# Performance work log

Measured on AMD Instinct MI355X. Metric: run time of the kernel, lower is better.

## Reference

```python
import jax, jax.numpy as jnp
import numpy as np
from jax import lax

# dims from the TED skeleton used by speech2affective_gestures
N, T, J, C = 256, 1024, 9, 3      # batch, frames, directed edges (graph1 nodes), coords
K1, K2 = 5, 3                     # spatial partitions of A1, A2
F1, F2 = 16, 16                   # st_gcn output channels
NUM_PARTS, MAX_EDGES = 3, 3       # body parts, edges per part
BODY_PARTS = np.array([[0, 1, 2], [3, 4, 5], [6, 7, 8]])  # body_parts_edge_idx
EPS = 1e-5
LEAK = 0.01


def conv2d_nchw(x, w):
    kh = w.shape[2]
    return lax.conv_general_dilated(x, w, (1, 1), ((kh // 2, kh // 2), (0, 0)),
                                    dimension_numbers=("NCHW", "OIHW", "NCHW"))


def conv1d_nch(x, w):
    k = w.shape[2]
    return lax.conv_general_dilated(x, w, (1,), ((k // 2, k // 2),),
                                    dimension_numbers=("NCH", "OIH", "NCH"))


def bn1d(x, w, b, m, v):
    # inference-mode BatchNorm1d over channel axis 1 of (N, C, T)
    scale = w / jnp.sqrt(v + EPS)
    return x * scale[None, :, None] + (b - m * scale)[None, :, None]


def leaky(x):
    return jnp.where(x > 0, x, LEAK * x)


def setup_inputs() -> dict:
    key = jax.random.key(0)
    ks = jax.random.split(key, 12)
    s = 0.05
    return {
        "poses": jax.random.normal(ks[0], (N, T, J * C), jnp.float32),
        "A1": jax.random.uniform(ks[1], (K1, J, J), jnp.float32) / J,
        "A2": jax.random.uniform(ks[2], (K2, NUM_PARTS, NUM_PARTS), jnp.float32) / NUM_PARTS,
        "W1": jax.random.normal(ks[3], (F1 * K1, C, 9, 1), jnp.float32) * s,
        "b1": jnp.zeros((F1 * K1,), jnp.float32),
        "W2": jax.random.normal(ks[4], (F2 * K2, MAX_EDGES * F1, 9, 1), jnp.float32) * s,
        "b2": jnp.zeros((F2 * K2,), jnp.float32),
        "Wc1": jax.random.normal(ks[5], (16, F2 * NUM_PARTS, 5), jnp.float32) * s,
        "bc1": jnp.zeros((16,), jnp.float32),
        "bn1_w": jnp.ones((16,), jnp.float32), "bn1_b": jnp.zeros((16,), jnp.float32),
        "bn1_m": jnp.zeros((16,), jnp.float32), "bn1_v": jnp.ones((16,), jnp.float32),
        "Wc2": jax.random.normal(ks[6], (8, 16, 3), jnp.float32) * s,
        "bc2": jnp.zeros((8,), jnp.float32),
        "bn2_w": jnp.ones((8,), jnp.float32), "bn2_b": jnp.zeros((8,), jnp.float32),
        "bn2_m": jnp.zeros((8,), jnp.float32), "bn2_v": jnp.ones((8,), jnp.float32),
    }


def reference(poses, A1, A2, W1, b1, W2, b2, Wc1, bc1, bn1_w, bn1_b, bn1_m, bn1_v,
              Wc2, bc2, bn2_w, bn2_b, bn2_m, bn2_v):
    n, t, jc = poses.shape
    x = jnp.transpose(poses.reshape(n, t, J, C), (0, 3, 1, 2))  # (n, 3, t, 9)

    # st_gcn1: temporal conv -> split K partitions -> graph contraction with A1
    y = conv2d_nchw(x, W1) + b1[None, :, None, None]            # (n, K1*F1, t, 9)
    y = y.reshape(n, K1, F1, t, J)
    feat1 = jnp.einsum("nkctv,kvw->nctw", y, A1)                # (n, 16, t, 9)

    # body-part gather/pack: feat2_in channel layout is (c slow, edge fast)
    g = feat1[:, :, :, BODY_PARTS]                              # (n, 16, t, parts, edges)
    feat2_in = jnp.transpose(g, (0, 1, 4, 2, 3)).reshape(n, F1 * MAX_EDGES, t, NUM_PARTS)

    # st_gcn2
    y2 = conv2d_nchw(feat2_in, W2) + b2[None, :, None, None]    # (n, K2*F2, t, 3)
    y2 = y2.reshape(n, K2, F2, t, NUM_PARTS)
    feat2 = jnp.einsum("nkctv,kvw->nctw", y2, A2)               # (n, 16, t, 3)

    # flatten (c, v) with c slow -> (n, 48, t)
    feat3_in = jnp.transpose(feat2, (0, 1, 3, 2)).reshape(n, F2 * NUM_PARTS, t)

    h = leaky(bn1d(conv1d_nch(feat3_in, Wc1) + bc1[None, :, None], bn1_w, bn1_b, bn1_m, bn1_v))
    h = leaky(bn1d(conv1d_nch(h, Wc2) + bc2[None, :, None], bn2_w, bn2_b, bn2_m, bn2_v))
    return jnp.transpose(h, (0, 2, 1))                          # (n, t, 8)
```

## Files before the change

### kernel.cpp

```cpp
#include <hip/hip_runtime.h>

namespace {
constexpr int T_ = 1024;
constexpr int NBATCH = 256;

constexpr int WFB_OFF    = 0;
constexpr int WFC_OFF    = 82944;
constexpr int WFD_OFF    = 221184;
constexpr int WBIG_OFF   = 231424;
constexpr int WFE_OFF    = 252928;
constexpr int BIASB_OFF  = 254976;
constexpr int BIASC_OFF  = 255552;
constexpr int BIASD_OFF  = 255744;
constexpr int BIASBIG_OFF= 255808;
constexpr int BIASE_OFF  = 255872;
constexpr int WCOMP_OFF  = 262144;

constexpr int R0 = 41472;
constexpr int R1 = R0 + 69120;
constexpr int R2 = R1 + 5120;
constexpr int R3 = R2 + 1024;
constexpr int R4 = R3 + 29952;
constexpr int R5 = R4 + 144;
constexpr int R6 = R5 + 48;
constexpr int R7 = R6 + 16;
constexpr int R8 = R7 + 8;

constexpr int SLAB_OFF  = 0;
constexpr int H1_OFF    = 18688;
constexpr int TT_FX     = 50;
constexpr int FXF2IN    = 0;
constexpr int FXF3      = FXF2IN + 72 * 320;
constexpr int FXSLAB    = FXF3 + 68 * 144;
constexpr int FXH1      = FXSLAB;
constexpr int SMEM_FUSE = FXSLAB + 72 * 80;
static_assert(SMEM_FUSE <= 65536, "fused LDS");

typedef __attribute__((ext_vector_type(8))) short short8v;
typedef __attribute__((ext_vector_type(4))) float f32x4;

__device__ inline unsigned short f2b(float f) {
  union { float f; unsigned u; } v; v.f = f;
  unsigned r = (v.u + 0x7FFFu + ((v.u >> 16) & 1u)) >> 16;
  return (unsigned short)r;
}
__device__ inline float b2f(unsigned short u) {
  union { unsigned u; float f; } v; v.u = ((unsigned)u) << 16;
  return v.f;
}
__device__ inline int fx_f2in_byte(int row, int slot, int within) {
  return FXF2IN + row * 320 + ((slot ^ ((row >> 2) & 3)) << 4) + within;
}
}

__global__ __launch_bounds__(256) void prep1_kernel(
    const float* __restrict__ A1, const float* __restrict__ A2,
    const float* __restrict__ W1, const float* __restrict__ b1,
    const float* __restrict__ W2, const float* __restrict__ b2,
    const float* __restrict__ Wc1, const float* __restrict__ bc1,
    const float* __restrict__ bn1w, const float* __restrict__ bn1b,
    const float* __restrict__ bn1m, const float* __restrict__ bn1v,
    const float* __restrict__ Wc2, const float* __restrict__ bc2,
    const float* __restrict__ bn2w, const float* __restrict__ bn2b,
    const float* __restrict__ bn2m, const float* __restrict__ bn2v,
    unsigned char* __restrict__ ws) {
  unsigned short* wfB = (unsigned short*)(ws + WFB_OFF);
  unsigned short* wfC = (unsigned short*)(ws + WFC_OFF);
  unsigned short* wfD = (unsigned short*)(ws + WFD_OFF);
  unsigned short* wfE = (unsigned short*)(ws + WFE_OFF);
  float* biasB = (float*)(ws + BIASB_OFF);
  float* biasC = (float*)(ws + BIASC_OFF);
  float* biasD = (float*)(ws + BIASD_OFF);
  float* biasE = (float*)(ws + BIASE_OFF);
  float* wcomp = (float*)(ws + WCOMP_OFF);
  for (int idx = blockIdx.x * 256 + threadIdx.x; idx < R8; idx += gridDim.x * 256) {
    if (idx < R0) {
      int ncol = idx / 288, k = idx - ncol * 288;
      int dh = k >> 5, mm = k & 31;
      float val = 0.f;
      if (mm < 27) {
        int v = mm / 3, ci = mm - v * 3;
        int p = ncol / 48, rr = ncol - p * 48, c = rr / 3, e = rr - c * 3;
        int w = p * 3 + e;
        for (int k5 = 0; k5 < 5; ++k5)
          val += W1[(k5 * 16 + c) * 27 + ci * 9 + dh] * A1[k5 * 81 + v * 9 + w];
      }
      wfB[idx] = f2b(val);
    } else if (idx < R1) {
      int i2 = idx - R0;
      int nc = i2 / 1440, k = i2 - nc * 1440;
      int dh = k / 160, off = k - dh * 160;
      float val = 0.f;
      if (off < 144) {
        int p = off / 48, ci2 = off - p * 48;
        int c2 = nc / 3, w2 = nc - c2 * 3;
        for (int k2 = 0; k2 < 3; ++k2)
          val += W2[(k2 * 16 + c2) * 432 + ci2 * 9 + dh] * A2[k2 * 9 + p * 3 + w2];
      }
      wfC[i2] = f2b(val);
    } else if (idx < R2) {
      int i3 = idx - R1;
      int o3 = i3 / 320, k = i3 - o3 * 320;
      int d = k >> 6, nc = k & 63;
      float val = 0.f;
      if (nc < 48) {
        float s1 = bn1w[o3] * rsqrtf(bn1v[o3] + 1e-5f);
        val = Wc1[o3 * 240 + nc * 5 + d] * s1;
      }
      wfD[i3] = f2b(val);
    } else if (idx < R3) {
      int i4 = idx - R2;
      int o4 = i4 >> 6, k = i4 & 63;
      float val = 0.f;
      if (o4 < 8 && k < 48) {
        int d = k >> 4, ci = k & 15;
        float s2 = bn2w[o4] * rsqrtf(bn2v[o4] + 1e-5f);
        val = Wc2[(o4 * 16 + ci) * 3 + d] * s2;
      }
      wfE[i4] = f2b(val);
    } else if (idx < R4) {
      int i5 = idx - R3;
      int o3 = i5 / 1872, rem = i5 - o3 * 1872;
      int dh2 = rem / 144, ncol = rem - dh2 * 144;
      int p = ncol / 48, ci2 = ncol - p * 48;
      float s1 = bn1w[o3] * rsqrtf(bn1v[o3] + 1e-5f);
      float acc = 0.f;
      for (int d = 0; d < 5; ++d) {
        int dh = dh2 - d;
        if (dh < 0 || dh > 8) continue;
        float wd = 0.f;
        for (int nc = 0; nc < 48; ++nc) {
          int c2 = nc / 3, w2 = nc - c2 * 3;
          float wc = 0.f;
          for (int k2 = 0; k2 < 3; ++k2)
            wc += W2[(k2 * 16 + c2) * 432 + ci2 * 9 + dh] * A2[k2 * 9 + p * 3 + w2];
          wd += Wc1[o3 * 240 + nc * 5 + d] * wc;
        }
        acc += wd * s1;
      }
      wcomp[i5] = acc;
    } else if (idx < R5) {
      int ib = idx - R4;
      int p = ib / 48, rr = ib - p * 48, c = rr / 3, e = rr - c * 3;
      int w = p * 3 + e;
      float val = 0.f;
      for (int k5 = 0; k5 < 5; ++k5)
        for (int v = 0; v < 9; ++v)
          val += b1[k5 * 16 + c] * A1[k5 * 81 + v * 9 + w];
      biasB[ib] = val;
    } else if (idx < R6) {
      int nc = idx - R5, c2 = nc / 3, w2 = nc - c2 * 3;
      float val = 0.f;
      for (int k2 = 0; k2 < 3; ++k2)
        for (int p = 0; p < 3; ++p)
          val += b2[k2 * 16 + c2] * A2[k2 * 9 + p * 3 + w2];
      biasC[nc] = val;
    } else if (idx < R7) {
      int o3 = idx - R6;
      float s1 = bn1w[o3] * rsqrtf(bn1v[o3] + 1e-5f);
      biasD[o3] = bc1[o3] * s1 + bn1b[o3] - bn1m[o3] * s1;
    } else {
      int o4 = idx - R7;
      float s2 = bn2w[o4] * rsqrtf(bn2v[o4] + 1e-5f);
      biasE[o4] = bc2[o4] * s2 + bn2b[o4] - bn2m[o4] * s2;
    }
  }
}

__global__ __launch_bounds__(256) void prep2_kernel(
    const float* __restrict__ Wc1, const float* __restrict__ bn1w,
    const float* __restrict__ bn1v, unsigned char* __restrict__ ws) {
  __shared__ float stgf[48 * 288];
  __shared__ float wl[1872];
  __shared__ float pr[256];
  __shared__ float pbias[192];
  const int dt = blockIdx.x, o3 = blockIdx.y;
  const int tid = threadIdx.x;
  const int m1 = tid & 31, p = tid >> 5;
  const unsigned short* wfB = (const unsigned short*)(ws + WFB_OFF);
  const float* wcomp = (const float*)(ws + WCOMP_OFF);
  unsigned short* wBIG = (unsigned short*)(ws + WBIG_OFF);

  for (int i = tid; i < 1872; i += 256) wl[i] = wcomp[o3 * 1872 + i];

  const int lo = (dt - 8) > 0 ? (dt - 8) : 0;
  const int hi = (dt < 12) ? dt : 12;
  float acc = 0.f;
  for (int c = 0; c < 3; ++c) {
    __syncthreads();
    for (int i = tid; i < 48 * 288; i += 256)
      stgf[i] = b2f(wfB[c * 13824 + i]);
    __syncthreads();
    for (int dh2 = lo; dh2 <= hi; ++dh2) {
      const int dh1 = dt - dh2;
      const float* wr = wl + dh2 * 144 + c * 48 + p * 6;
      const float* br = stgf + (p * 6) * 288 + dh1 * 32 + m1;
#pragma unroll
      for (int j = 0; j < 6; ++j)
        acc += wr[j] * br[j * 288];
    }
  }
  pr[tid] = acc;
  __syncthreads();
  if (tid < 32) {
    float s = pr[tid];
#pragma unroll
    for (int pp = 1; pp < 8; ++pp) s += pr[pp * 32 + tid];
    wBIG[o3 * 672 + dt * 32 + tid] = f2b(s);
  }
  if (dt == 0) {
    if (tid < 144) {
      float s = 0.f;
      for (int dh2 = 0; dh2 < 13; ++dh2) s += wl[dh2 * 144 + tid];
      pbias[tid] = s * ((const float*)(ws + BIASB_OFF))[tid];
    } else if (tid < 192) {
      int nc = tid - 144;
      float s1 = bn1w[o3] * rsqrtf(bn1v[o3] + 1e-5f);
      float s = 0.f;
#pragma unroll
      for (int d = 0; d < 5; ++d) s += Wc1[o3 * 240 + nc * 5 + d];
      pbias[tid] = s * s1 * ((const float*)(ws + BIASC_OFF))[nc];
    }
    __syncthreads();
    if (tid == 0) {
      float accb = ((const float*)(ws + BIASD_OFF))[o3];
      for (int i = 0; i < 192; ++i) accb += pbias[i];
      ((float*)(ws + BIASBIG_OFF))[o3] = accb;
    }
  }
}

__global__ __launch_bounds__(256, 3) void fused_kernel(
    const float* __restrict__ poses,
    const float* __restrict__ Wc2, const float* __restrict__ bc2,
    const float* __restrict__ bn2w, const float* __restrict__ bn2b,
    const float* __restrict__ bn2m, const float* __restrict__ bn2v,
    const unsigned char* __restrict__ ws, float* __restrict__ out) {
  __shared__ __attribute__((aligned(16))) unsigned char smem[SMEM_FUSE];
  const int tid = threadIdx.x;
  const int n = blockIdx.y;
  const int w = tid >> 6, l = tid & 63, lrow = l & 15, q = l >> 4, q8 = q * 8;

  if (blockIdx.x < 4) {
    const int t0 = blockIdx.x * 256;
    {
      unsigned* s32 = (unsigned*)(smem + SLAB_OFF);
      for (int idx = tid; idx < 292 * 16; idx += 256) {
        int r = idx >> 4, mi = idx & 15, m0 = mi * 2;
        int t = t0 - 18 + r;
        float v0 = 0.f, v1 = 0.f;
        if (t >= 0 && t < T_) {
          const float* src = poses + ((long)n * T_ + t) * 27;
          if (m0 < 27) v0 = src[m0];
          if (m0 + 1 < 27) v1 = src[m0 + 1];
        }
        s32[idx] = (unsigned)f2b(v0) | ((unsigned)f2b(v1) << 16);
      }
    }

    const float bb = ((const float*)(ws + BIASBIG_OFF))[lrow];
    const float be = ((const float*)(ws + BIASE_OFF))[lrow & 7];
    const unsigned short* wbg = (const unsigned short*)(ws + WBIG_OFF);
    short8v B[21];
#pragma unroll
    for (int dt = 0; dt < 21; ++dt)
      B[dt] = *(const short8v*)(wbg + lrow * 672 + dt * 32 + q8);
    const unsigned short* wfe = (const unsigned short*)(ws + WFE_OFF);
    const short8v E0 = *(const short8v*)(wfe + lrow * 64 + q8);
    const short8v E1 = *(const short8v*)(wfe + lrow * 64 + 32 + q8);
    __syncthreads();

#pragma unroll
    for (int i = 0; i < 5; ++i) {
      if (i == 4 && w != 0) continue;
      const int mt = (i < 4) ? (w + i * 4) : 16;
      const int sbase = SLAB_OFF + (mt * 16 + lrow) * 64 + q8 * 2;
      f32x4 c0 = {0.f, 0.f, 0.f, 0.f}, c1 = {0.f, 0.f, 0.f, 0.f};
      short8v a[7];
#pragma unroll
      for (int dt = 0; dt < 7; ++dt) a[dt] = *(const short8v*)(smem + sbase + dt * 64);
#pragma unroll
      for (int dt = 0; dt < 7; ++dt) {
        if (dt & 1) c1 = __builtin_amdgcn_mfma_f32_16x16x32_bf16(a[dt], B[dt], c1, 0, 0, 0);
        else        c0 = __builtin_amdgcn_mfma_f32_16x16x32_bf16(a[dt], B[dt], c0, 0, 0, 0);
      }
#pragma unroll
      for (int dt = 0; dt < 7; ++dt) a[dt] = *(const short8v*)(smem + sbase + (7 + dt) * 64);
#pragma unroll
      for (int dt = 0; dt < 7; ++dt) {
        if (dt & 1) c1 = __builtin_amdgcn_mfma_f32_16x16x32_bf16(a[dt], B[7 + dt], c1, 0, 0, 0);
        else        c0 = __builtin_amdgcn_mfma_f32_16x16x32_bf16(a[dt], B[7 + dt], c0, 0, 0, 0);
      }
#pragma unroll
      for (int dt = 0; dt < 7; ++dt) a[dt] = *(const short8v*)(smem + sbase + (14 + dt) * 64);
#pragma unroll
      for (int dt = 0; dt < 7; ++dt) {
        if (dt & 1) c1 = __builtin_amdgcn_mfma_f32_16x16x32_bf16(a[dt], B[14 + dt], c1, 0, 0, 0);
        else        c0 = __builtin_amdgcn_mfma_f32_16x16x32_bf16(a[dt], B[14 + dt], c0, 0, 0, 0);
      }
      const int hbase = H1_OFF + (mt * 16 + q * 4) * 32 + lrow * 2;
#pragma unroll
      for (int jj = 0; jj < 4; ++jj) {
        float x = c0[jj] + c1[jj] + bb;
        float h = x > 0.f ? x : 0.01f * x;
        *(unsigned short*)(smem + hbase + jj * 32) = f2b(h);
      }
    }
    __syncthreads();

#pragma unroll
    for (int i = 0; i < 4; ++i) {
      const int mte = w + i * 4;
      const int abase = H1_OFF + (7 + mte * 16 + lrow) * 32 + q8 * 2;
      short8v A0v = *(const short8v*)(smem + abase);
      short8v A1v = *(const short8v*)(smem + abase + 64);
      f32x4 acc = {0.f, 0.f, 0.f, 0.f};
      acc = __builtin_amdgcn_mfma_f32_16x16x32_bf16(A0v, E0, acc, 0, 0, 0);
      acc = __builtin_amdgcn_mfma_f32_16x16x32_bf16(A1v, E1, acc, 0, 0, 0);
      if (lrow < 8) {
        const int tb = t0 + mte * 16 + q * 4;
#pragma unroll
        for (int jj = 0; jj < 4; ++jj) {
          const int t = tb + jj;
          if (t >= 7 && t < 1017) {
            float x = acc[jj] + be;
            out[((long)n * T_ + t) * 8 + lrow] = x > 0.f ? x : 0.01f * x;
          }
        }
      }
    }
    return;
  }

  const unsigned short* wfB = (const unsigned short*)(ws + WFB_OFF);
  const unsigned short* wfC = (const unsigned short*)(ws + WFC_OFF);
  const unsigned short* wfD = (const unsigned short*)(ws + WFD_OFF);
  const float* biasB = (const float*)(ws + BIASB_OFF);
  const float* biasC = (const float*)(ws + BIASC_OFF);
  const float* biasD = (const float*)(ws + BIASD_OFF);
  const int e = blockIdx.x - 4;
  const int t0 = e ? (T_ - TT_FX) : 0;

  {
    unsigned* slab32 = (unsigned*)(smem + FXSLAB);
    for (int it = tid; it < 72 * 20; it += 256) {
      int r = it / 20, mi = it - r * 20;
      int t = t0 - 11 + r;
      int m0 = mi * 2;
      float v0 = 0.f, v1 = 0.f;
      if (t >= 0 && t < T_) {
        const float* src = poses + ((long)n * T_ + t) * 27;
        if (m0 < 27) v0 = src[m0];
        if (m0 + 1 < 27) v1 = src[m0 + 1];
      }
      slab32[it] = (unsigned)f2b(v0) | ((unsigned)f2b(v1) << 16);
    }
    for (int it = tid; it < 64 * 8; it += 256) {
      int r = it >> 3, u = it & 7;
      int s = 18 + (u >> 2);
      *(unsigned*)(smem + fx_f2in_byte(r, s, (u & 3) * 4)) = 0;
    }
    for (int it = tid; it < 8 * 80; it += 256) {
      int r = 64 + it / 80, u = it - (it / 80) * 80;
      *(unsigned*)(smem + FXF2IN + r * 320 + u * 4) = 0;
    }
    for (int it = tid; it < 68 * 8 + 12 * 24; it += 256) {
      if (it < 68 * 8) {
        int r = it >> 3, u = it & 7;
        *(unsigned*)(smem + FXF3 + r * 144 + 96 + u * 4) = 0;
      } else {
        int k2 = it - 68 * 8;
        int r = 56 + k2 / 24, u = k2 - (k2 / 24) * 24;
        *(unsigned*)(smem + FXF3 + r * 144 + u * 4) = 0;
      }
    }
  }
  __syncthreads();

  {
    const int ntS = (w == 0) ? 0 : (2 * w + 1);
    const int ntN = (w == 0) ? 3 : 2;
#pragma unroll
    for (int ni = 0; ni < 3; ++ni) {
      if (ni < ntN) {
        const int nt = ntS + ni;
        short8v b[9];
#pragma unroll
        for (int dh = 0; dh < 9; ++dh)
          b[dh] = *(const short8v*)(wfB + (nt * 16 + lrow) * 288 + dh * 32 + q8);
        const int ncol = nt * 16 + lrow;
        const float bias = biasB[ncol];
#pragma unroll
        for (int mt = 0; mt < 4; ++mt) {
          short8v a[9];
#pragma unroll
          for (int dh = 0; dh < 9; ++dh)
            a[dh] = *(const short8v*)(smem + FXSLAB + ((mt * 16 + lrow + dh) * 40 + q8) * 2);
          f32x4 c0 = {0.f, 0.f, 0.f, 0.f}, c1 = {0.f, 0.f, 0.f, 0.f};
#pragma unroll
          for (int dh = 0; dh < 9; ++dh) {
            if (dh & 1) c1 = __builtin_amdgcn_mfma_f32_16x16x32_bf16(a[dh], b[dh], c1, 0, 0, 0);
            else        c0 = __builtin_amdgcn_mfma_f32_16x16x32_bf16(a[dh], b[dh], c0, 0, 0, 0);
          }
#pragma unroll
          for (int jj = 0; jj < 4; ++jj) {
            const int r = mt * 16 + q * 4 + jj;
            const int t = t0 - 7 + r;
            float v = (t >= 0 && t < T_) ? c0[jj] + c1[jj] + bias : 0.f;
            *(unsigned short*)(smem + fx_f2in_byte(r, ncol >> 3, (ncol & 7) * 2)) = f2b(v);
          }
        }
      }
    }
  }
  __syncthreads();

  if (w < 3) {
    const int ncol2 = w * 16 + lrow;
    const float bias = biasC[ncol2];
    f32x4 acc[4];
#pragma unroll
    for (int mt = 0; mt < 4; ++mt) acc[mt] = {0.f, 0.f, 0.f, 0.f};
#pragma unroll
    for (int g = 0; g < 5; ++g) {
      short8v b[9];
#pragma unroll
      for (int i = 0; i < 9; ++i) {
        const int kf = g * 9 + i, dh = kf / 5, kkl = kf % 5;
        b[i] = *(const short8v*)(wfC + ncol2 * 1440 + dh * 160 + kkl * 32 + q8);
      }
#pragma unroll
      for (int mt = 0; mt < 4; ++mt) {
        short8v a[9];
#pragma unroll
        for (int i = 0; i < 9; ++i) {
          const int kf = g * 9 + i, dh = kf / 5, kkl = kf % 5;
          a[i] = *(const short8v*)(smem + fx_f2in_byte(mt * 16 + lrow + dh, 4 * kkl + q, 0));
        }
#pragma unroll
        for (int i = 0; i < 9; ++i)
          acc[mt] = __builtin_amdgcn_mfma_f32_16x16x32_bf16(a[i], b[i], acc[mt], 0, 0, 0);
      }
    }
#pragma unroll
    for (int mt = 0; mt < 4; ++mt) {
#pragma unroll
      for (int jj = 0; jj < 4; ++jj) {
        const int rt3 = mt * 16 + q * 4 + jj;
        if (rt3 < 56) {
          const int t = t0 - 3 + rt3;
          float v = (t >= 0 && t < T_) ? acc[mt][jj] + bias : 0.f;
          *(unsigned short*)(smem + FXF3 + rt3 * 144 + ncol2 * 2) = f2b(v);
        }
      }
    }
  }
  __syncthreads();

  {
    const int arow = w * 16 + lrow;
    short8v a[10], b[10];
#pragma unroll
    for (int kf = 0; kf < 10; ++kf) {
      const int d = kf >> 1, kkl = kf & 1;
      b[kf] = *(const short8v*)(wfD + lrow * 320 + d * 64 + kkl * 32 + q8);
      a[kf] = *(const short8v*)(smem + FXF3 + (arow + d) * 144 + (kkl * 32 + q8) * 2);
    }
    f32x4 c0 = {0.f, 0.f, 0.f, 0.f}, c1 = {0.f, 0.f, 0.f, 0.f};
#pragma unroll
    for (int kf = 0; kf < 10; ++kf) {
      if (kf & 1) c1 = __builtin_amdgcn_mfma_f32_16x16x32_bf16(a[kf], b[kf], c1, 0, 0, 0);
      else        c0 = __builtin_amdgcn_mfma_f32_16x16x32_bf16(a[kf], b[kf], c0, 0, 0, 0);
    }
    const float bias = biasD[lrow];
#pragma unroll
    for (int jj = 0; jj < 4; ++jj) {
      const int rh = w * 16 + q * 4 + jj;
      if (rh < 52) {
        const int t = t0 - 1 + rh;
        float v = 0.f;
        if (t >= 0 && t < T_) {
          float x = c0[jj] + c1[jj] + bias;
          v = x > 0.f ? x : 0.01f * x;
        }
        *(float*)(smem + FXH1 + (rh * 17 + lrow) * 4) = v;
      }
    }
  }
  __syncthreads();

  for (int it = tid; it < TT_FX * 8; it += 256) {
    int rt = it >> 3, o4 = it & 7;
    int t = t0 + rt;
    if (t >= T_) continue;
    if (e ? (t < 1017) : (t >= 7)) continue;
    float s2 = bn2w[o4] * rsqrtf(bn2v[o4] + 1e-5f);
    float t2 = bc2[o4] * s2 + bn2b[o4] - bn2m[o4] * s2;
    float acc = 0.f;
#pragma unroll
    for (int d = 0; d < 3; ++d) {
      const float* hr = (const float*)(smem + FXH1 + (rt + d) * 68);
#pragma unroll
      for (int ci = 0; ci < 16; ++ci)
        acc = fmaf(hr[ci], Wc2[(o4 * 16 + ci) * 3 + d], acc);
    }
    float v = acc * s2 + t2;
    out[((long)n * T_ + t) * 8 + o4] = v > 0.f ? v : 0.01f * v;
  }
}

extern "C" void kernel_launch(void* const* d_in, const int* in_sizes, int n_in,
                              void* d_out, int out_size, void* d_ws, size_t ws_size,
                              hipStream_t stream) {
  (void)in_sizes; (void)n_in; (void)out_size; (void)ws_size;
  const float* poses = (const float*)d_in[0];
  const float* A1    = (const float*)d_in[1];
  const float* A2    = (const float*)d_in[2];
  const float* W1    = (const float*)d_in[3];
  const float* b1    = (const float*)d_in[4];
  const float* W2    = (const float*)d_in[5];
  const float* b2    = (const float*)d_in[6];
  const float* Wc1   = (const float*)d_in[7];
  const float* bc1   = (const float*)d_in[8];
  const float* bn1w  = (const float*)d_in[9];
  const float* bn1b  = (const float*)d_in[10];
  const float* bn1m  = (const float*)d_in[11];
  const float* bn1v  = (const float*)d_in[12];
  const float* Wc2   = (const float*)d_in[13];
  const float* bc2   = (const float*)d_in[14];
  const float* bn2w  = (const float*)d_in[15];
  const float* bn2b  = (const float*)d_in[16];
  const float* bn2m  = (const float*)d_in[17];
  const float* bn2v  = (const float*)d_in[18];
  float* out = (float*)d_out;
  unsigned char* ws = (unsigned char*)d_ws;

  hipLaunchKernelGGL(prep1_kernel, dim3(144), dim3(256), 0, stream,
                     A1, A2, W1, b1, W2, b2, Wc1, bc1, bn1w, bn1b, bn1m, bn1v,
                     Wc2, bc2, bn2w, bn2b, bn2m, bn2v, ws);
  hipLaunchKernelGGL(prep2_kernel, dim3(21, 16), dim3(256), 0, stream,
                     Wc1, bn1w, bn1v, ws);
  hipLaunchKernelGGL(fused_kernel, dim3(6, NBATCH), dim3(256), 0, stream,
                     poses, Wc2, bc2, bn2w, bn2b, bn2m, bn2v, ws, out);
}
```

Before: 78.84 us.

## Halve main-block time tile and vectorize pose slab loads with float4

```diff
diff --git a/kernel.cpp b/kernel.cpp
--- a/kernel.cpp
+++ b/kernel.cpp
@@ -26,18 +26,19 @@
 constexpr int R7 = R6 + 16;
 constexpr int R8 = R7 + 8;
 
-constexpr int SLAB_OFF  = 0;
-constexpr int H1_OFF    = 18688;
-constexpr int TT_FX     = 50;
-constexpr int FXF2IN    = 0;
-constexpr int FXF3      = FXF2IN + 72 * 320;
-constexpr int FXSLAB    = FXF3 + 68 * 144;
-constexpr int FXH1      = FXSLAB;
+constexpr int MSLAB = 0;
+constexpr int MH1   = 10496;
+constexpr int TT_FX = 50;
+constexpr int FXF2IN = 0;
+constexpr int FXF3   = FXF2IN + 72 * 320;
+constexpr int FXSLAB = FXF3 + 68 * 144;
+constexpr int FXH1   = FXSLAB;
 constexpr int SMEM_FUSE = FXSLAB + 72 * 80;
 static_assert(SMEM_FUSE <= 65536, "fused LDS");
 
 typedef __attribute__((ext_vector_type(8))) short short8v;
 typedef __attribute__((ext_vector_type(4))) float f32x4;
+typedef float f4u __attribute__((ext_vector_type(4), aligned(4)));
 
 __device__ inline unsigned short f2b(float f) {
   union { float f; unsigned u; } v; v.f = f;
@@ -230,7 +231,7 @@
   }
 }
 
-__global__ __launch_bounds__(256, 3) void fused_kernel(
+__global__ __launch_bounds__(256, 4) void fused_kernel(
     const float* __restrict__ poses,
     const float* __restrict__ Wc2, const float* __restrict__ bc2,
     const float* __restrict__ bn2w, const float* __restrict__ bn2b,
@@ -241,20 +242,49 @@
   const int n = blockIdx.y;
   const int w = tid >> 6, l = tid & 63, lrow = l & 15, q = l >> 4, q8 = q * 8;
 
-  if (blockIdx.x < 4) {
-    const int t0 = blockIdx.x * 256;
+  if (blockIdx.x < 8) {
+    const int t0 = blockIdx.x * 128;
+    const int lo = (t0 - 18 < 0) ? 0 : (t0 - 18);
+    const int hi = (t0 + 146 > T_) ? T_ : (t0 + 146);
+    const int rlo = lo - (t0 - 18), rhi = hi - (t0 - 18);
     {
-      unsigned* s32 = (unsigned*)(smem + SLAB_OFF);
-      for (int idx = tid; idx < 292 * 16; idx += 256) {
-        int r = idx >> 4, mi = idx & 15, m0 = mi * 2;
-        int t = t0 - 18 + r;
-        float v0 = 0.f, v1 = 0.f;
-        if (t >= 0 && t < T_) {
-          const float* src = poses + ((long)n * T_ + t) * 27;
-          if (m0 < 27) v0 = src[m0];
-          if (m0 + 1 < 27) v1 = src[m0 + 1];
-        }
-        s32[idx] = (unsigned)f2b(v0) | ((unsigned)f2b(v1) << 16);
+      for (int idx = tid; idx < 164 * 3; idx += 256) {
+        int r = idx / 3, u = idx - (idx / 3) * 3;
+        if (u == 0) *(unsigned short*)(smem + MSLAB + r * 64 + 54) = 0;
+        else        *(unsigned*)(smem + MSLAB + r * 64 + (13 + u) * 4) = 0;
+      }
+      const int nz = rlo + (164 - rhi);
+      for (int idx = tid; idx < nz * 16; idx += 256) {
+        int z = idx >> 4, u = idx & 15;
+        int r = (z < rlo) ? z : (rhi + z - rlo);
+        *(unsigned*)(smem + MSLAB + r * 64 + u * 4) = 0;
+      }
+      const float* pbase = poses + (long)n * T_ * 27;
+      const int gs = (lo * 27) & ~3;
+      const int ge = hi * 27;
+      const int glo = lo * 27;
+      for (int i4 = tid; gs + i4 * 4 < ge; i4 += 256) {
+        const int g0 = gs + i4 * 4;
+        if (g0 >= glo && g0 + 3 < ge) {
+          f4u v4 = *(const f4u*)(pbase + g0);
+#pragma unroll
+          for (int j = 0; j < 4; ++j) {
+            int g = g0 + j;
+            int t = g / 27, m = g - t * 27;
+            int r = t - (t0 - 18);
+            *(unsigned short*)(smem + MSLAB + r * 64 + m * 2) = f2b(v4[j]);
+          }
+        } else {
+#pragma unroll
+          for (int j = 0; j < 4; ++j) {
+            int g = g0 + j;
+            if (g >= glo && g < ge) {
+              int t = g / 27, m = g - t * 27;
+              int r = t - (t0 - 18);
+              *(unsigned short*)(smem + MSLAB + r * 64 + m * 2) = f2b(pbase[g]);
+            }
+          }
+        }
       }
     }
 
@@ -271,10 +301,10 @@
     __syncthreads();
 
 #pragma unroll
-    for (int i = 0; i < 5; ++i) {
-      if (i == 4 && w != 0) continue;
-      const int mt = (i < 4) ? (w + i * 4) : 16;
-      const int sbase = SLAB_OFF + (mt * 16 + lrow) * 64 + q8 * 2;
+    for (int i = 0; i < 3; ++i) {
+      if (i == 2 && w != 0) continue;
+      const int mt = (i < 2) ? (w + i * 4) : 8;
+      const int sbase = MSLAB + (mt * 16 + lrow) * 64 + q8 * 2;
       f32x4 c0 = {0.f, 0.f, 0.f, 0.f}, c1 = {0.f, 0.f, 0.f, 0.f};
       short8v a[7];
 #pragma unroll
@@ -298,7 +328,7 @@
         if (dt & 1) c1 = __builtin_amdgcn_mfma_f32_16x16x32_bf16(a[dt], B[14 + dt], c1, 0, 0, 0);
         else        c0 = __builtin_amdgcn_mfma_f32_16x16x32_bf16(a[dt], B[14 + dt], c0, 0, 0, 0);
       }
-      const int hbase = H1_OFF + (mt * 16 + q * 4) * 32 + lrow * 2;
+      const int hbase = MH1 + (mt * 16 + q * 4) * 32 + lrow * 2;
 #pragma unroll
       for (int jj = 0; jj < 4; ++jj) {
         float x = c0[jj] + c1[jj] + bb;
@@ -309,9 +339,9 @@
     __syncthreads();
 
 #pragma unroll
-    for (int i = 0; i < 4; ++i) {
+    for (int i = 0; i < 2; ++i) {
       const int mte = w + i * 4;
-      const int abase = H1_OFF + (7 + mte * 16 + lrow) * 32 + q8 * 2;
+      const int abase = MH1 + (7 + mte * 16 + lrow) * 32 + q8 * 2;
       short8v A0v = *(const short8v*)(smem + abase);
       short8v A1v = *(const short8v*)(smem + abase + 64);
       f32x4 acc = {0.f, 0.f, 0.f, 0.f};
@@ -338,7 +368,7 @@
   const float* biasB = (const float*)(ws + BIASB_OFF);
   const float* biasC = (const float*)(ws + BIASC_OFF);
   const float* biasD = (const float*)(ws + BIASD_OFF);
-  const int e = blockIdx.x - 4;
+  const int e = blockIdx.x - 8;
   const int t0 = e ? (T_ - TT_FX) : 0;
 
   {
@@ -540,6 +570,6 @@
                      Wc2, bc2, bn2w, bn2b, bn2m, bn2v, ws);
   hipLaunchKernelGGL(prep2_kernel, dim3(21, 16), dim3(256), 0, stream,
                      Wc1, bn1w, bn1v, ws);
-  hipLaunchKernelGGL(fused_kernel, dim3(6, NBATCH), dim3(256), 0, stream,
+  hipLaunchKernelGGL(fused_kernel, dim3(10, NBATCH), dim3(256), 0, stream,
                      poses, Wc2, bc2, bn2w, bn2b, bn2m, bn2v, ws, out);
 }
```

Result: slower. 82.82 us (+5.0%).

## Split fused kernel into small-LDS main kernel and separate edge fixup kernel

Applied to the files above, without the earlier changes.

```diff
diff --git a/kernel.cpp b/kernel.cpp
--- a/kernel.cpp
+++ b/kernel.cpp
@@ -26,15 +26,17 @@
 constexpr int R7 = R6 + 16;
 constexpr int R8 = R7 + 8;
 
-constexpr int SLAB_OFF  = 0;
-constexpr int H1_OFF    = 18688;
-constexpr int TT_FX     = 50;
-constexpr int FXF2IN    = 0;
-constexpr int FXF3      = FXF2IN + 72 * 320;
-constexpr int FXSLAB    = FXF3 + 68 * 144;
-constexpr int FXH1      = FXSLAB;
-constexpr int SMEM_FUSE = FXSLAB + 72 * 80;
-static_assert(SMEM_FUSE <= 65536, "fused LDS");
+constexpr int MSLAB = 0;
+constexpr int MH1   = 10496;
+constexpr int SMEM_MAIN = 15104;
+
+constexpr int TT_FX = 50;
+constexpr int FXF2IN = 0;
+constexpr int FXF3   = FXF2IN + 72 * 320;
+constexpr int FXSLAB = FXF3 + 68 * 144;
+constexpr int FXH1   = FXSLAB;
+constexpr int SMEM_FX = FXSLAB + 72 * 80;
+static_assert(SMEM_FX <= 65536, "fixup LDS");
 
 typedef __attribute__((ext_vector_type(8))) short short8v;
 typedef __attribute__((ext_vector_type(4))) float f32x4;
@@ -230,116 +232,125 @@
   }
 }
 
-__global__ __launch_bounds__(256, 3) void fused_kernel(
+__global__ __launch_bounds__(256, 2) void main_kernel(
+    const float* __restrict__ poses, const unsigned char* __restrict__ ws,
+    float* __restrict__ out) {
+  __shared__ __attribute__((aligned(16))) unsigned char smem[SMEM_MAIN];
+  const int tid = threadIdx.x;
+  const int n = blockIdx.y;
+  const int t0 = blockIdx.x * 128;
+  const int w = tid >> 6, l = tid & 63, lrow = l & 15, q = l >> 4, q8 = q * 8;
+
+  {
+    unsigned* s32 = (unsigned*)(smem + MSLAB);
+    for (int idx = tid; idx < 164 * 16; idx += 256) {
+      int r = idx >> 4, mi = idx & 15, m0 = mi * 2;
+      int t = t0 - 18 + r;
+      float v0 = 0.f, v1 = 0.f;
+      if (m0 < 27 && t >= 0 && t < T_) {
+        const float* src = poses + ((long)n * T_ + t) * 27;
+        v0 = src[m0];
+        if (m0 + 1 < 27) v1 = src[m0 + 1];
+      }
+      s32[idx] = (unsigned)f2b(v0) | ((unsigned)f2b(v1) << 16);
+    }
+  }
+
+  const float bb = ((const float*)(ws + BIASBIG_OFF))[lrow];
+  const float be = ((const float*)(ws + BIASE_OFF))[lrow & 7];
+  const unsigned short* wbg = (const unsigned short*)(ws + WBIG_OFF);
+  short8v B[21];
+#pragma unroll
+  for (int dt = 0; dt < 21; ++dt)
+    B[dt] = *(const short8v*)(wbg + lrow * 672 + dt * 32 + q8);
+  const unsigned short* wfe = (const unsigned short*)(ws + WFE_OFF);
+  short8v E0 = *(const short8v*)(wfe + lrow * 64 + q8);
+  short8v E1 = *(const short8v*)(wfe + lrow * 64 + 32 + q8);
+#pragma unroll
+  for (int dt = 0; dt < 21; ++dt) asm volatile("" : "+v"(B[dt]));
+  asm volatile("" : "+v"(E0));
+  asm volatile("" : "+v"(E1));
+  __syncthreads();
+
+#pragma unroll
+  for (int i = 0; i < 3; ++i) {
+    if (i == 2 && w != 0) continue;
+    const int mt = (i < 2) ? (w + i * 4) : 8;
+    const int sbase = MSLAB + (mt * 16 + lrow) * 64 + q8 * 2;
+    f32x4 c0 = {0.f, 0.f, 0.f, 0.f}, c1 = {0.f, 0.f, 0.f, 0.f};
+    short8v a[7];
+#pragma unroll
+    for (int dt = 0; dt < 7; ++dt) a[dt] = *(const short8v*)(smem + sbase + dt * 64);
+#pragma unroll
+    for (int dt = 0; dt < 7; ++dt) {
+      if (dt & 1) c1 = __builtin_amdgcn_mfma_f32_16x16x32_bf16(a[dt], B[dt], c1, 0, 0, 0);
+      else        c0 = __builtin_amdgcn_mfma_f32_16x16x32_bf16(a[dt], B[dt], c0, 0, 0, 0);
+    }
+#pragma unroll
+    for (int dt = 0; dt < 7; ++dt) a[dt] = *(const short8v*)(smem + sbase + (7 + dt) * 64);
+#pragma unroll
+    for (int dt = 0; dt < 7; ++dt) {
+      if (dt & 1) c1 = __builtin_amdgcn_mfma_f32_16x16x32_bf16(a[dt], B[7 + dt], c1, 0, 0, 0);
+      else        c0 = __builtin_amdgcn_mfma_f32_16x16x32_bf16(a[dt], B[7 + dt], c0, 0, 0, 0);
+    }
+#pragma unroll
+    for (int dt = 0; dt < 7; ++dt) a[dt] = *(const short8v*)(smem + sbase + (14 + dt) * 64);
+#pragma unroll
+    for (int dt = 0; dt < 7; ++dt) {
+      if (dt & 1) c1 = __builtin_amdgcn_mfma_f32_16x16x32_bf16(a[dt], B[14 + dt], c1, 0, 0, 0);
+      else        c0 = __builtin_amdgcn_mfma_f32_16x16x32_bf16(a[dt], B[14 + dt], c0, 0, 0, 0);
+    }
+    const int hbase = MH1 + (mt * 16 + q * 4) * 32 + lrow * 2;
+#pragma unroll
+    for (int jj = 0; jj < 4; ++jj) {
+      float x = c0[jj] + c1[jj] + bb;
+      float h = x > 0.f ? x : 0.01f * x;
+      *(unsigned short*)(smem + hbase + jj * 32) = f2b(h);
+    }
+  }
+  __syncthreads();
+
+#pragma unroll
+  for (int i = 0; i < 2; ++i) {
+    const int mte = w + i * 4;
+    const int abase = MH1 + (7 + mte * 16 + lrow) * 32 + q8 * 2;
+    short8v A0v = *(const short8v*)(smem + abase);
+    short8v A1v = *(const short8v*)(smem + abase + 64);
+    f32x4 acc = {0.f, 0.f, 0.f, 0.f};
+    acc = __builtin_amdgcn_mfma_f32_16x16x32_bf16(A0v, E0, acc, 0, 0, 0);
+    acc = __builtin_amdgcn_mfma_f32_16x16x32_bf16(A1v, E1, acc, 0, 0, 0);
+    if (lrow < 8) {
+      const int tb = t0 + mte * 16 + q * 4;
+#pragma unroll
+      for (int jj = 0; jj < 4; ++jj) {
+        const int t = tb + jj;
+        if (t >= 7 && t < 1017) {
+          float x = acc[jj] + be;
+          out[((long)n * T_ + t) * 8 + lrow] = x > 0.f ? x : 0.01f * x;
+        }
+      }
+    }
+  }
+}
+
+__global__ __launch_bounds__(256, 2) void fixup_kernel(
     const float* __restrict__ poses,
     const float* __restrict__ Wc2, const float* __restrict__ bc2,
     const float* __restrict__ bn2w, const float* __restrict__ bn2b,
     const float* __restrict__ bn2m, const float* __restrict__ bn2v,
     const unsigned char* __restrict__ ws, float* __restrict__ out) {
-  __shared__ __attribute__((aligned(16))) unsigned char smem[SMEM_FUSE];
+  __shared__ __attribute__((aligned(16))) unsigned char smem[SMEM_FX];
   const int tid = threadIdx.x;
   const int n = blockIdx.y;
+  const int e = blockIdx.x;
+  const int t0 = e ? (T_ - TT_FX) : 0;
   const int w = tid >> 6, l = tid & 63, lrow = l & 15, q = l >> 4, q8 = q * 8;
-
-  if (blockIdx.x < 4) {
-    const int t0 = blockIdx.x * 256;
-    {
-      unsigned* s32 = (unsigned*)(smem + SLAB_OFF);
-      for (int idx = tid; idx < 292 * 16; idx += 256) {
-        int r = idx >> 4, mi = idx & 15, m0 = mi * 2;
-        int t = t0 - 18 + r;
-        float v0 = 0.f, v1 = 0.f;
-        if (t >= 0 && t < T_) {
-          const float* src = poses + ((long)n * T_ + t) * 27;
-          if (m0 < 27) v0 = src[m0];
-          if (m0 + 1 < 27) v1 = src[m0 + 1];
-        }
-        s32[idx] = (unsigned)f2b(v0) | ((unsigned)f2b(v1) << 16);
-      }
-    }
-
-    const float bb = ((const float*)(ws + BIASBIG_OFF))[lrow];
-    const float be = ((const float*)(ws + BIASE_OFF))[lrow & 7];
-    const unsigned short* wbg = (const unsigned short*)(ws + WBIG_OFF);
-    short8v B[21];
-#pragma unroll
-    for (int dt = 0; dt < 21; ++dt)
-      B[dt] = *(const short8v*)(wbg + lrow * 672 + dt * 32 + q8);
-    const unsigned short* wfe = (const unsigned short*)(ws + WFE_OFF);
-    const short8v E0 = *(const short8v*)(wfe + lrow * 64 + q8);
-    const short8v E1 = *(const short8v*)(wfe + lrow * 64 + 32 + q8);
-    __syncthreads();
-
-#pragma unroll
-    for (int i = 0; i < 5; ++i) {
-      if (i == 4 && w != 0) continue;
-      const int mt = (i < 4) ? (w + i * 4) : 16;
-      const int sbase = SLAB_OFF + (mt * 16 + lrow) * 64 + q8 * 2;
-      f32x4 c0 = {0.f, 0.f, 0.f, 0.f}, c1 = {0.f, 0.f, 0.f, 0.f};
-      short8v a[7];
-#pragma unroll
-      for (int dt = 0; dt < 7; ++dt) a[dt] = *(const short8v*)(smem + sbase + dt * 64);
-#pragma unroll
-      for (int dt = 0; dt < 7; ++dt) {
-        if (dt & 1) c1 = __builtin_amdgcn_mfma_f32_16x16x32_bf16(a[dt], B[dt], c1, 0, 0, 0);
-        else        c0 = __builtin_amdgcn_mfma_f32_16x16x32_bf16(a[dt], B[dt], c0, 0, 0, 0);
-      }
-#pragma unroll
-      for (int dt = 0; dt < 7; ++dt) a[dt] = *(const short8v*)(smem + sbase + (7 + dt) * 64);
-#pragma unroll
-      for (int dt = 0; dt < 7; ++dt) {
-        if (dt & 1) c1 = __builtin_amdgcn_mfma_f32_16x16x32_bf16(a[dt], B[7 + dt], c1, 0, 0, 0);
-        else        c0 = __builtin_amdgcn_mfma_f32_16x16x32_bf16(a[dt], B[7 + dt], c0, 0, 0, 0);
-      }
-#pragma unroll
-      for (int dt = 0; dt < 7; ++dt) a[dt] = *(const short8v*)(smem + sbase + (14 + dt) * 64);
-#pragma unroll
-      for (int dt = 0; dt < 7; ++dt) {
-        if (dt & 1) c1 = __builtin_amdgcn_mfma_f32_16x16x32_bf16(a[dt], B[14 + dt], c1, 0, 0, 0);
-        else        c0 = __builtin_amdgcn_mfma_f32_16x16x32_bf16(a[dt], B[14 + dt], c0, 0, 0, 0);
-      }
-      const int hbase = H1_OFF + (mt * 16 + q * 4) * 32 + lrow * 2;
-#pragma unroll
-      for (int jj = 0; jj < 4; ++jj) {
-        float x = c0[jj] + c1[jj] + bb;
-        float h = x > 0.f ? x : 0.01f * x;
-        *(unsigned short*)(smem + hbase + jj * 32) = f2b(h);
-      }
-    }
-    __syncthreads();
-
-#pragma unroll
-    for (int i = 0; i < 4; ++i) {
-      const int mte = w + i * 4;
-      const int abase = H1_OFF + (7 + mte * 16 + lrow) * 32 + q8 * 2;
-      short8v A0v = *(const short8v*)(smem + abase);
-      short8v A1v = *(const short8v*)(smem + abase + 64);
-      f32x4 acc = {0.f, 0.f, 0.f, 0.f};
-      acc = __builtin_amdgcn_mfma_f32_16x16x32_bf16(A0v, E0, acc, 0, 0, 0);
-      acc = __builtin_amdgcn_mfma_f32_16x16x32_bf16(A1v, E1, acc, 0, 0, 0);
-      if (lrow < 8) {
-        const int tb = t0 + mte * 16 + q * 4;
-#pragma unroll
-        for (int jj = 0; jj < 4; ++jj) {
-          const int t = tb + jj;
-          if (t >= 7 && t < 1017) {
-            float x = acc[jj] + be;
-            out[((long)n * T_ + t) * 8 + lrow] = x > 0.f ? x : 0.01f * x;
-          }
-        }
-      }
-    }
-    return;
-  }
-
   const unsigned short* wfB = (const unsigned short*)(ws + WFB_OFF);
   const unsigned short* wfC = (const unsigned short*)(ws + WFC_OFF);
   const unsigned short* wfD = (const unsigned short*)(ws + WFD_OFF);
   const float* biasB = (const float*)(ws + BIASB_OFF);
   const float* biasC = (const float*)(ws + BIASC_OFF);
   const float* biasD = (const float*)(ws + BIASD_OFF);
-  const int e = blockIdx.x - 4;
-  const int t0 = e ? (T_ - TT_FX) : 0;
 
   {
     unsigned* slab32 = (unsigned*)(smem + FXSLAB);
@@ -540,6 +551,8 @@
                      Wc2, bc2, bn2w, bn2b, bn2m, bn2v, ws);
   hipLaunchKernelGGL(prep2_kernel, dim3(21, 16), dim3(256), 0, stream,
                      Wc1, bn1w, bn1v, ws);
-  hipLaunchKernelGGL(fused_kernel, dim3(6, NBATCH), dim3(256), 0, stream,
+  hipLaunchKernelGGL(fixup_kernel, dim3(2, NBATCH), dim3(256), 0, stream,
                      poses, Wc2, bc2, bn2w, bn2b, bn2m, bn2v, ws, out);
-}
+  hipLaunchKernelGGL(main_kernel, dim3(8, NBATCH), dim3(256), 0, stream,
+                     poses, ws, out);
+}
```

Result: slower. 87.11 us (+10.5%).
